# Kernel optimization log

Measured on AMD Instinct MI355X. Metric: run time of the kernel, lower is better.

Reference implementation:

```python
import jax, jax.numpy as jnp
import numpy as np

V = 50000   # words_num
D = 128     # embedding_dim
B = 2048    # batch
P = 20      # max Huffman path length


def setup_inputs() -> dict:
    key = jax.random.key(0)
    k1, k2, k3, k4, k5 = jax.random.split(key, 5)
    inputs_vector = jax.random.uniform(k1, (B, V), dtype=jnp.float32)
    path_nodes_indices = jax.random.randint(k2, (B, P), 0, V)
    huffman_codes = jax.random.randint(k3, (B, P), 0, 2).astype(jnp.float32)
    mask = jnp.ones((B, P), dtype=jnp.float32)
    # learned params, torch nn.Linear weight layout [out, in], kaiming-uniform-ish scale
    W_emb = jax.random.uniform(k4, (D, V), dtype=jnp.float32, minval=-1.0, maxval=1.0) / np.sqrt(V)
    W_cls = jax.random.uniform(k5, (V, D), dtype=jnp.float32, minval=-1.0, maxval=1.0) / np.sqrt(D)
    return {
        "inputs_vector": inputs_vector,
        "W_emb": W_emb,
        "W_cls": W_cls,
        "path_nodes_indices": path_nodes_indices,
        "huffman_codes": huffman_codes,
        "mask": mask,
    }


def _bce_with_logits(logits, targets):
    # numerically stable, elementwise (reduction='none')
    return jnp.maximum(logits, 0.0) - logits * targets + jnp.log1p(jnp.exp(-jnp.abs(logits)))


def reference(inputs_vector, W_emb, W_cls, path_nodes_indices, huffman_codes, mask):
    x = inputs_vector @ W_emb.T              # [B, D]  embedding Linear (no bias)
    logits_full = x @ W_cls.T                # [B, V]  full-vocab cls matmul (as in source)
    logits = jnp.take_along_axis(logits_full, path_nodes_indices, axis=1)  # [B, P]
    loss = _bce_with_logits(logits, huffman_codes)  # [B, P]
    masked_loss = loss * mask
    per_sample = masked_loss.sum(axis=-1) / mask.sum(axis=-1)  # [B]
    return per_sample.mean()
```

## Files before the change

kernel.cpp:

```cpp
#include <hip/hip_runtime.h>
#include <hip/hip_bf16.h>

#define V 50000
#define D 128
#define B 2048
#define P 20

#define BM 128
#define BK 32
#define NSPLIT 48
#define KC 1056
#define VPAD (NSPLIT * KC)
#define NMT (B / BM)

typedef float  f32x4  __attribute__((ext_vector_type(4)));
typedef short  bf16x8 __attribute__((ext_vector_type(8)));
typedef unsigned int uint4v __attribute__((ext_vector_type(4)));

__device__ __forceinline__ unsigned int pk2(float a, float b) {
    return (__float_as_uint(b) & 0xFFFF0000u) | (__float_as_uint(a) >> 16);
}
__device__ __forceinline__ unsigned short f2bf(float f) {
    unsigned int u = __float_as_uint(f);
    return (unsigned short)((u + 0x7FFFu + ((u >> 16) & 1u)) >> 16);
}
__device__ __forceinline__ bf16x8 pack8(f32x4 lo, f32x4 hi) {
    union { uint4v u; bf16x8 h; } r;
    r.u.x = pk2(lo[0], lo[1]); r.u.y = pk2(lo[2], lo[3]);
    r.u.z = pk2(hi[0], hi[1]); r.u.w = pk2(hi[2], hi[3]);
    return r.h;
}
__device__ __forceinline__ void gload_lds16(const void* g, void* l) {
    __builtin_amdgcn_global_load_lds(
        (const __attribute__((address_space(1))) unsigned int*)g,
        (__attribute__((address_space(3))) unsigned int*)l, 16, 0, 0);
}

__global__ __launch_bounds__(256)
void w2v_wcast(const float* __restrict__ Wemb, unsigned short* __restrict__ Wb) {
    const size_t t = (size_t)blockIdx.x * 256 + threadIdx.x;
    const size_t n = (size_t)D * VPAD / 8;
    if (t >= n) return;
    const size_t base = t * 8;
    const int d = (int)(base / VPAD);
    const int k = (int)(base % VPAD);
    uint4v u = {0u, 0u, 0u, 0u};
    if (k + 8 <= V) {
        const f32x4* src = reinterpret_cast<const f32x4*>(Wemb + (size_t)d * V + k);
        f32x4 v0 = src[0], v1 = src[1];
        u.x = pk2(v0[0], v0[1]); u.y = pk2(v0[2], v0[3]);
        u.z = pk2(v1[0], v1[1]); u.w = pk2(v1[2], v1[3]);
    }
    *reinterpret_cast<uint4v*>(Wb + (size_t)d * VPAD + k) = u;
}

template<int FAST>
__global__ __launch_bounds__(256, 3)
void w2v_gemm(const float* __restrict__ Ain, const void* __restrict__ Wsrc,
              void* __restrict__ part) {
    __shared__ char smem[49152];

    const int i   = blockIdx.x;
    const int xcd = i & 7;
    const int q   = i >> 3;
    const int s   = xcd * 6 + (q >> 4);
    const int mt  = q & 15;
    const int m0  = mt * BM;
    const int k0  = s * KC;
    const int k1  = (k0 + KC < V) ? (k0 + KC) : V;
    const int nfull  = (k1 - k0) >> 5;
    const int ktail  = (k1 - k0) & 31;
    const int nsteps = nfull + (ktail ? 1 : 0);

    const int tid  = threadIdx.x;
    const int lane = tid & 63;
    const int wid  = tid >> 6;
    const int w32  = wid * 32;
    const int fr   = lane & 15;
    const int kg4  = lane >> 4;

    f32x4 acc[2][8] = {};

    const int arow = w32 + (lane >> 3);
    const int csrc = (lane & 7) ^ (lane >> 3);
    const float* aSrc = Ain + (size_t)(m0 + arow) * V + csrc * 4;

    const unsigned short* WbP = (const unsigned short*)Wsrc;
    const float*          WfP = (const float*)Wsrc;
    const int wrow = w32 + (lane >> 2);
    const unsigned short* wSrc = WbP + (size_t)wrow * VPAD + (lane & 3) * 8;

    auto stageA = [&](int buf, int ks) {
#pragma unroll
        for (int j = 0; j < 4; ++j)
            gload_lds16(aSrc + ks + (size_t)j * 8 * V,
                        smem + buf * 16384 + w32 * 128 + j * 1024);
    };
    auto stageW = [&](int buf, int ks) {
        if (FAST) {
#pragma unroll
            for (int j = 0; j < 2; ++j)
                gload_lds16(wSrc + ks + (size_t)j * 16 * VPAD,
                            smem + 32768 + buf * 8192 + w32 * 64 + j * 1024);
        } else {
#pragma unroll
            for (int j = 0; j < 2; ++j) {
                const int slot = tid + j * 256;
                const int d    = slot >> 2;
                const int cp   = slot & 3;
                const int kg   = ks + cp * 8;
                uint4v u = {0u, 0u, 0u, 0u};
                if (kg + 8 <= V) {
                    const f32x4* sp = reinterpret_cast<const f32x4*>(WfP + (size_t)d * V + kg);
                    f32x4 v0 = sp[0], v1 = sp[1];
                    u.x = pk2(v0[0], v0[1]); u.y = pk2(v0[2], v0[3]);
                    u.z = pk2(v1[0], v1[1]); u.w = pk2(v1[2], v1[3]);
                }
                *reinterpret_cast<uint4v*>(smem + 32768 + buf * 8192 + d * 64 + cp * 16) = u;
            }
        }
    };
    auto stageAtail = [&](int buf, int ks) {
#pragma unroll
        for (int j = 0; j < 4; ++j) {
            const int slot = tid + j * 256;
            const int row  = slot >> 3;
            const int cp   = slot & 7;
            const int cd   = cp ^ (row & 7);
            const int kg   = ks + cd * 4;
            f32x4 v = {0.f, 0.f, 0.f, 0.f};
            if (kg + 4 <= V)
                v = *reinterpret_cast<const f32x4*>(Ain + (size_t)(m0 + row) * V + kg);
            *reinterpret_cast<f32x4*>(smem + buf * 16384 + row * 128 + cp * 16) = v;
        }
    };

    int cur = 0;
    if (nfull > 0) stageA(0, k0); else stageAtail(0, k0);
    stageW(0, k0);
    __syncthreads();

    for (int t = 0; t < nsteps; ++t) {
        const int tn = t + 1;
        if (tn < nsteps) {
            const int ksn = k0 + tn * 32;
            if (tn < nfull) stageA(cur ^ 1, ksn); else stageAtail(cur ^ 1, ksn);
            stageW(cur ^ 1, ksn);
        }
        const char* Ab = smem + cur * 16384;
        const char* Wl = smem + 32768 + cur * 8192;
        bf16x8 af[2];
        const int c0 = (2 * kg4) ^ (fr & 7);
#pragma unroll
        for (int m = 0; m < 2; ++m) {
            const char* rb = Ab + (w32 + m * 16 + fr) * 128;
            f32x4 lo = *reinterpret_cast<const f32x4*>(rb + c0 * 16);
            f32x4 hi = *reinterpret_cast<const f32x4*>(rb + (c0 ^ 1) * 16);
            af[m] = pack8(lo, hi);
        }
#pragma unroll
        for (int n = 0; n < 8; ++n) {
            const bf16x8 wf = *reinterpret_cast<const bf16x8*>(Wl + (n * 16 + fr) * 64 + kg4 * 16);
            acc[0][n] = __builtin_amdgcn_mfma_f32_16x16x32_bf16(af[0], wf, acc[0][n], 0, 0, 0);
            acc[1][n] = __builtin_amdgcn_mfma_f32_16x16x32_bf16(af[1], wf, acc[1][n], 0, 0, 0);
        }
        __syncthreads();
        cur ^= 1;
    }

    if (!FAST) {
        float* outp = (float*)part;
#pragma unroll
        for (int m = 0; m < 2; ++m) {
            const int r0 = m0 + w32 + m * 16 + kg4 * 4;
#pragma unroll
            for (int n = 0; n < 8; ++n) {
                const int c = n * 16 + fr;
#pragma unroll
                for (int jj = 0; jj < 4; ++jj)
                    atomicAdd(&outp[(size_t)(r0 + jj) * D + c], acc[m][n][jj]);
            }
        }
        return;
    }
    unsigned short* Cs = (unsigned short*)smem;
#pragma unroll
    for (int m = 0; m < 2; ++m) {
        const int r0 = w32 + m * 16 + kg4 * 4;
#pragma unroll
        for (int n = 0; n < 8; ++n) {
            const int c = n * 16 + fr;
#pragma unroll
            for (int jj = 0; jj < 4; ++jj)
                Cs[(r0 + jj) * 128 + c] = f2bf(acc[m][n][jj]);
        }
    }
    __syncthreads();
    char* dstb = (char*)part + ((size_t)s * B + m0) * (D * 2);
#pragma unroll
    for (int it = 0; it < 8; ++it) {
        const int off = (it * 256 + tid) * 16;
        uint4v v = *reinterpret_cast<const uint4v*>(smem + off);
        *reinterpret_cast<uint4v*>(dstb + off) = v;
    }
}

__global__ __launch_bounds__(256)
void w2v_loss(const void* __restrict__ part, int part_bf16,
              const float* __restrict__ Wcls, const int* __restrict__ pathIdx,
              const float* __restrict__ codes, const float* __restrict__ mask,
              float* __restrict__ out) {
    const int lane = threadIdx.x & 63;
    const int wid  = threadIdx.x >> 6;
    const int b    = blockIdx.x * 4 + wid;

    float x0 = 0.f, x1 = 0.f;
    if (part_bf16) {
        const unsigned* pb = (const unsigned*)part;
#pragma unroll 8
        for (int s = 0; s < NSPLIT; ++s) {
            unsigned u = pb[((size_t)s * B + b) * 64 + lane];
            x0 += __uint_as_float(u << 16);
            x1 += __uint_as_float(u & 0xFFFF0000u);
        }
    } else {
        const float* pf = (const float*)part;
        const float2 v = *reinterpret_cast<const float2*>(&pf[(size_t)b * D + lane * 2]);
        x0 = v.x; x1 = v.y;
    }

    float lsum = 0.f, msum = 0.f;
#pragma unroll
    for (int p = 0; p < P; ++p) {
        int node = pathIdx[b * P + p];
        const float2 w = *reinterpret_cast<const float2*>(&Wcls[(size_t)node * D + lane * 2]);
        float d = x0 * w.x + x1 * w.y;
#pragma unroll
        for (int off = 1; off < 64; off <<= 1)
            d += __shfl_xor(d, off, 64);
        float t  = codes[b * P + p];
        float mm = mask[b * P + p];
        float loss = fmaxf(d, 0.f) - d * t + log1pf(__expf(-fabsf(d)));
        lsum += loss * mm;
        msum += mm;
    }
    float per = (msum > 0.f) ? (lsum / msum) : 0.f;

    __shared__ float wsum[4];
    if (lane == 0) wsum[wid] = per;
    __syncthreads();
    if (threadIdx.x == 0) {
        float ssum = wsum[0] + wsum[1] + wsum[2] + wsum[3];
        atomicAdd(out, ssum * (1.0f / (float)B));
    }
}

extern "C" void kernel_launch(void* const* d_in, const int* in_sizes, int n_in,
                              void* d_out, int out_size, void* d_ws, size_t ws_size,
                              hipStream_t stream) {
    const float* inputs = (const float*)d_in[0];
    const float* W_emb  = (const float*)d_in[1];
    const float* W_cls  = (const float*)d_in[2];
    const int*   path   = (const int*)  d_in[3];
    const float* codes  = (const float*)d_in[4];
    const float* mask   = (const float*)d_in[5];
    float* out = (float*)d_out;

    hipMemsetAsync(d_out, 0, sizeof(float), stream);

    const size_t wb_bytes  = (size_t)D * VPAD * 2;
    const size_t part_off  = (wb_bytes + 255) & ~(size_t)255;
    const size_t part_need = part_off + (size_t)NSPLIT * B * D * 2;

    if (ws_size >= part_need) {
        unsigned short* Wb = (unsigned short*)d_ws;
        char* partp = (char*)d_ws + part_off;
        w2v_wcast<<<dim3((unsigned)((size_t)D * VPAD / 8 / 256)), dim3(256), 0, stream>>>(W_emb, Wb);
        w2v_gemm<1><<<dim3(NMT * NSPLIT), dim3(256), 0, stream>>>(inputs, Wb, partp);
        w2v_loss<<<dim3(B / 4), dim3(256), 0, stream>>>(partp, 1, W_cls, path, codes, mask, out);
    } else {
        hipMemsetAsync(d_ws, 0, (size_t)B * D * sizeof(float), stream);
        w2v_gemm<0><<<dim3(NMT * NSPLIT), dim3(256), 0, stream>>>(inputs, W_emb, d_ws);
        w2v_loss<<<dim3(B / 4), dim3(256), 0, stream>>>(d_ws, 0, W_cls, path, codes, mask, out);
    }
}
```

Before: 145.0 us.

## Replace async double-buffered GEMM staging with single-buffer BK=64 register-staged loads

Drops the global_load_lds double-buffered pipeline in the split-K GEMM. A is now loaded through registers, converted to bf16 once at staging time, and stored into a padded LDS tile with stride 72. The K step is doubled to 64 and tail handling is unified. This removes the per-MFMA fp32-to-bf16 packing and halves the A footprint in LDS. In exchange it loses the overlap of global loads with compute, since the single buffer serializes loading and MFMA work behind two barriers per step.

New measurement: 171.3 us. 1.18x slower.

```diff
diff --git a/kernel.cpp b/kernel.cpp
--- a/kernel.cpp
+++ b/kernel.cpp
@@ -7,7 +7,8 @@
 #define P 20
 
 #define BM 128
-#define BK 32
+#define BK 64
+#define LDK 72
 #define NSPLIT 48
 #define KC 1056
 #define VPAD (NSPLIT * KC)
@@ -16,6 +17,7 @@
 typedef float  f32x4  __attribute__((ext_vector_type(4)));
 typedef short  bf16x8 __attribute__((ext_vector_type(8)));
 typedef unsigned int uint4v __attribute__((ext_vector_type(4)));
+typedef unsigned int uint2v __attribute__((ext_vector_type(2)));
 
 __device__ __forceinline__ unsigned int pk2(float a, float b) {
     return (__float_as_uint(b) & 0xFFFF0000u) | (__float_as_uint(a) >> 16);
@@ -23,17 +25,6 @@
 __device__ __forceinline__ unsigned short f2bf(float f) {
     unsigned int u = __float_as_uint(f);
     return (unsigned short)((u + 0x7FFFu + ((u >> 16) & 1u)) >> 16);
-}
-__device__ __forceinline__ bf16x8 pack8(f32x4 lo, f32x4 hi) {
-    union { uint4v u; bf16x8 h; } r;
-    r.u.x = pk2(lo[0], lo[1]); r.u.y = pk2(lo[2], lo[3]);
-    r.u.z = pk2(hi[0], hi[1]); r.u.w = pk2(hi[2], hi[3]);
-    return r.h;
-}
-__device__ __forceinline__ void gload_lds16(const void* g, void* l) {
-    __builtin_amdgcn_global_load_lds(
-        (const __attribute__((address_space(1))) unsigned int*)g,
-        (__attribute__((address_space(3))) unsigned int*)l, 16, 0, 0);
 }
 
 __global__ __launch_bounds__(256)
@@ -58,7 +49,9 @@
 __global__ __launch_bounds__(256, 3)
 void w2v_gemm(const float* __restrict__ Ain, const void* __restrict__ Wsrc,
               void* __restrict__ part) {
-    __shared__ char smem[49152];
+    __shared__ unsigned short Sm[2 * BM * LDK];
+    unsigned short* As = Sm;
+    unsigned short* Ws = Sm + BM * LDK;
 
     const int i   = blockIdx.x;
     const int xcd = i & 7;
@@ -68,9 +61,7 @@
     const int m0  = mt * BM;
     const int k0  = s * KC;
     const int k1  = (k0 + KC < V) ? (k0 + KC) : V;
-    const int nfull  = (k1 - k0) >> 5;
-    const int ktail  = (k1 - k0) & 31;
-    const int nsteps = nfull + (ktail ? 1 : 0);
+    const int nsteps = (k1 - k0 + 63) >> 6;
 
     const int tid  = threadIdx.x;
     const int lane = tid & 63;
@@ -81,91 +72,63 @@
 
     f32x4 acc[2][8] = {};
 
-    const int arow = w32 + (lane >> 3);
-    const int csrc = (lane & 7) ^ (lane >> 3);
-    const float* aSrc = Ain + (size_t)(m0 + arow) * V + csrc * 4;
-
-    const unsigned short* WbP = (const unsigned short*)Wsrc;
-    const float*          WfP = (const float*)Wsrc;
-    const int wrow = w32 + (lane >> 2);
-    const unsigned short* wSrc = WbP + (size_t)wrow * VPAD + (lane & 3) * 8;
-
-    auto stageA = [&](int buf, int ks) {
-#pragma unroll
-        for (int j = 0; j < 4; ++j)
-            gload_lds16(aSrc + ks + (size_t)j * 8 * V,
-                        smem + buf * 16384 + w32 * 128 + j * 1024);
-    };
-    auto stageW = [&](int buf, int ks) {
-        if (FAST) {
-#pragma unroll
-            for (int j = 0; j < 2; ++j)
-                gload_lds16(wSrc + ks + (size_t)j * 16 * VPAD,
-                            smem + 32768 + buf * 8192 + w32 * 64 + j * 1024);
-        } else {
-#pragma unroll
-            for (int j = 0; j < 2; ++j) {
-                const int slot = tid + j * 256;
-                const int d    = slot >> 2;
-                const int cp   = slot & 3;
-                const int kg   = ks + cp * 8;
-                uint4v u = {0u, 0u, 0u, 0u};
+    const unsigned short* Wb = (const unsigned short*)Wsrc;
+    const float*          Wf = (const float*)Wsrc;
+
+    for (int t = 0; t < nsteps; ++t) {
+        const int ks = k0 + t * 64;
+
+#pragma unroll
+        for (int it = 0; it < 8; ++it) {
+            const int slot = tid + it * 256;
+            const int row  = slot >> 4;
+            const int kv   = slot & 15;
+            const int kg   = ks + kv * 4;
+            f32x4 v = {0.f, 0.f, 0.f, 0.f};
+            if (kg + 4 <= k1)
+                v = *reinterpret_cast<const f32x4*>(Ain + (size_t)(m0 + row) * V + kg);
+            uint2v u;
+            u.x = pk2(v[0], v[1]);
+            u.y = pk2(v[2], v[3]);
+            *reinterpret_cast<uint2v*>(&As[row * LDK + kv * 4]) = u;
+        }
+#pragma unroll
+        for (int it = 0; it < 4; ++it) {
+            const int slot = tid + it * 256;
+            const int d    = slot >> 3;
+            const int c8   = slot & 7;
+            const int kg   = ks + c8 * 8;
+            uint4v u;
+            if (FAST) {
+                u = *reinterpret_cast<const uint4v*>(Wb + (size_t)d * VPAD + kg);
+            } else {
+                u.x = 0u; u.y = 0u; u.z = 0u; u.w = 0u;
                 if (kg + 8 <= V) {
-                    const f32x4* sp = reinterpret_cast<const f32x4*>(WfP + (size_t)d * V + kg);
+                    const f32x4* sp = reinterpret_cast<const f32x4*>(Wf + (size_t)d * V + kg);
                     f32x4 v0 = sp[0], v1 = sp[1];
                     u.x = pk2(v0[0], v0[1]); u.y = pk2(v0[2], v0[3]);
                     u.z = pk2(v1[0], v1[1]); u.w = pk2(v1[2], v1[3]);
                 }
-                *reinterpret_cast<uint4v*>(smem + 32768 + buf * 8192 + d * 64 + cp * 16) = u;
             }
-        }
-    };
-    auto stageAtail = [&](int buf, int ks) {
-#pragma unroll
-        for (int j = 0; j < 4; ++j) {
-            const int slot = tid + j * 256;
-            const int row  = slot >> 3;
-            const int cp   = slot & 7;
-            const int cd   = cp ^ (row & 7);
-            const int kg   = ks + cd * 4;
-            f32x4 v = {0.f, 0.f, 0.f, 0.f};
-            if (kg + 4 <= V)
-                v = *reinterpret_cast<const f32x4*>(Ain + (size_t)(m0 + row) * V + kg);
-            *reinterpret_cast<f32x4*>(smem + buf * 16384 + row * 128 + cp * 16) = v;
-        }
-    };
-
-    int cur = 0;
-    if (nfull > 0) stageA(0, k0); else stageAtail(0, k0);
-    stageW(0, k0);
-    __syncthreads();
-
-    for (int t = 0; t < nsteps; ++t) {
-        const int tn = t + 1;
-        if (tn < nsteps) {
-            const int ksn = k0 + tn * 32;
-            if (tn < nfull) stageA(cur ^ 1, ksn); else stageAtail(cur ^ 1, ksn);
-            stageW(cur ^ 1, ksn);
-        }
-        const char* Ab = smem + cur * 16384;
-        const char* Wl = smem + 32768 + cur * 8192;
-        bf16x8 af[2];
-        const int c0 = (2 * kg4) ^ (fr & 7);
-#pragma unroll
-        for (int m = 0; m < 2; ++m) {
-            const char* rb = Ab + (w32 + m * 16 + fr) * 128;
-            f32x4 lo = *reinterpret_cast<const f32x4*>(rb + c0 * 16);
-            f32x4 hi = *reinterpret_cast<const f32x4*>(rb + (c0 ^ 1) * 16);
-            af[m] = pack8(lo, hi);
-        }
-#pragma unroll
-        for (int n = 0; n < 8; ++n) {
-            const bf16x8 wf = *reinterpret_cast<const bf16x8*>(Wl + (n * 16 + fr) * 64 + kg4 * 16);
-            acc[0][n] = __builtin_amdgcn_mfma_f32_16x16x32_bf16(af[0], wf, acc[0][n], 0, 0, 0);
-            acc[1][n] = __builtin_amdgcn_mfma_f32_16x16x32_bf16(af[1], wf, acc[1][n], 0, 0, 0);
+            *reinterpret_cast<uint4v*>(&Ws[d * LDK + c8 * 8]) = u;
         }
         __syncthreads();
-        cur ^= 1;
+
+#pragma unroll
+        for (int kk = 0; kk < BK; kk += 32) {
+            const int kfo = kk + kg4 * 8;
+            bf16x8 af[2];
+#pragma unroll
+            for (int m = 0; m < 2; ++m)
+                af[m] = *reinterpret_cast<const bf16x8*>(&As[(w32 + m * 16 + fr) * LDK + kfo]);
+#pragma unroll
+            for (int n = 0; n < 8; ++n) {
+                const bf16x8 wf = *reinterpret_cast<const bf16x8*>(&Ws[(n * 16 + fr) * LDK + kfo]);
+                acc[0][n] = __builtin_amdgcn_mfma_f32_16x16x32_bf16(af[0], wf, acc[0][n], 0, 0, 0);
+                acc[1][n] = __builtin_amdgcn_mfma_f32_16x16x32_bf16(af[1], wf, acc[1][n], 0, 0, 0);
+            }
+        }
+        __syncthreads();
     }
 
     if (!FAST) {
@@ -183,7 +146,7 @@
         }
         return;
     }
-    unsigned short* Cs = (unsigned short*)smem;
+    unsigned short* Cs = Sm;
 #pragma unroll
     for (int m = 0; m < 2; ++m) {
         const int r0 = w32 + m * 16 + kg4 * 4;
@@ -200,7 +163,7 @@
 #pragma unroll
     for (int it = 0; it < 8; ++it) {
         const int off = (it * 256 + tid) * 16;
-        uint4v v = *reinterpret_cast<const uint4v*>(smem + off);
+        uint4v v = *reinterpret_cast<const uint4v*>((char*)Sm + off);
         *reinterpret_cast<uint4v*>(dstb + off) = v;
     }
 }
```
